# Optimization experiments

Hardware: AMD Instinct MI355X
Metric: run time of the kernel (lower is better)

Reference implementation:

```python
import jax, jax.numpy as jnp
import numpy as np

D_MODEL = 2048
N_HEADS = 16
HEAD_DIM = D_MODEL // N_HEADS
ROPE_BASE = 10000.0
B, T = 2, 2048


def setup_inputs() -> dict:
    key = jax.random.key(0)
    k1, k2, k3 = jax.random.split(key, 3)
    s_in = 1.0 / np.sqrt(D_MODEL)
    x = jax.random.normal(k1, (B, T, D_MODEL), dtype=jnp.float32)
    Wqkv = jax.random.normal(k2, (3 * D_MODEL, D_MODEL), dtype=jnp.float32) * s_in
    bqkv = jnp.zeros((3 * D_MODEL,), dtype=jnp.float32)
    Wo = jax.random.normal(k3, (D_MODEL, D_MODEL), dtype=jnp.float32) * s_in
    bo = jnp.zeros((D_MODEL,), dtype=jnp.float32)
    return {"x": x, "Wqkv": Wqkv, "bqkv": bqkv, "Wo": Wo, "bo": bo}


def _rotate_half(x):
    # [x1,x2,x3,x4] -> [-x2,x1,-x4,x3] (interleaved pairs)
    x_even = x[..., 0::2]
    x_odd = x[..., 1::2]
    return jnp.stack((-x_odd, x_even), axis=-1).reshape(x.shape)


def _rope_cos_sin(seq_len, dtype):
    half = HEAD_DIM // 2
    inv_freq = 1.0 / (ROPE_BASE ** (jnp.arange(half, dtype=jnp.float32) / half))
    freqs = jnp.arange(seq_len, dtype=jnp.float32)[:, None] * inv_freq[None, :]  # (T, half)
    emb = jnp.repeat(freqs, 2, axis=-1)  # (T, D) interleaved
    cos = jnp.cos(emb).astype(dtype)[None, None]  # (1,1,T,D)
    sin = jnp.sin(emb).astype(dtype)[None, None]
    return cos, sin


def reference(x, Wqkv, bqkv, Wo, bo):
    b, t, c = x.shape
    qkv = jnp.einsum('btc,fc->btf', x, Wqkv) + bqkv  # (B,T,3C)
    q, k, v = jnp.split(qkv, 3, axis=-1)
    def to_heads(z):
        return z.reshape(b, t, N_HEADS, HEAD_DIM).transpose(0, 2, 1, 3)  # (B,H,T,D)
    q, k, v = to_heads(q), to_heads(k), to_heads(v)
    cos, sin = _rope_cos_sin(t, x.dtype)
    q = q * cos + _rotate_half(q) * sin
    k = k * cos + _rotate_half(k) * sin
    scale = 1.0 / jnp.sqrt(jnp.asarray(HEAD_DIM, dtype=x.dtype))
    scores = jnp.einsum('bhqd,bhkd->bhqk', q, k) * scale  # (B,H,T,T)
    causal = jnp.tril(jnp.ones((t, t), dtype=bool))
    scores = jnp.where(causal, scores, jnp.finfo(scores.dtype).min)
    attn = jax.nn.softmax(scores, axis=-1)
    out = jnp.einsum('bhqk,bhkd->bhqd', attn, v)  # (B,H,T,D)
    out = out.transpose(0, 2, 1, 3).reshape(b, t, c)
    return jnp.einsum('btc,oc->bto', out, Wo) + bo
```

## Files before the change

### kernel.cpp

```cpp
#include <hip/hip_runtime.h>

using f16 = _Float16;
typedef _Float16 h8 __attribute__((ext_vector_type(8)));
typedef _Float16 h4 __attribute__((ext_vector_type(4)));
typedef float f4 __attribute__((ext_vector_type(4)));
typedef unsigned int u32;
typedef unsigned long long u64;

#define DEVI static __device__ __forceinline__

DEVI f4 mfma16(h8 a, h8 b, f4 c) {
  return __builtin_amdgcn_mfma_f32_16x16x32_f16(a, b, c, 0, 0, 0);
}

DEVI void gl_lds16(const f16* g, f16* l) {
  __builtin_amdgcn_global_load_lds(
      (const __attribute__((address_space(1))) u32*)g,
      (__attribute__((address_space(3))) u32*)l, 16, 0, 0);
}

DEVI u32 pkh2(float a, float b) {
  union { f16 h[2]; u32 u; } x;
  x.h[0] = (f16)a; x.h[1] = (f16)b;
  return x.u;
}

typedef float fv4 __attribute__((ext_vector_type(4)));

__global__ __launch_bounds__(256) void k_cvt(const float* __restrict__ in,
                                             f16* __restrict__ out, int n4) {
  int i = blockIdx.x * 256 + threadIdx.x;
  if (i >= n4) return;
  fv4 v = ((const fv4*)in)[i];
  h4 o;
  o[0] = (f16)v[0]; o[1] = (f16)v[1]; o[2] = (f16)v[2]; o[3] = (f16)v[3];
  ((h4*)out)[i] = o;
}

__global__ __launch_bounds__(256) void k_rope_tbl(float* __restrict__ tbl) {
  int i = blockIdx.x * 256 + threadIdx.x;
  int t = i >> 6, d = i & 63;
  float invf = exp2f(-(float)d * (13.287712379549449f / 64.f));
  float a = (float)t * invf;
  tbl[2 * i]     = cosf(a);
  tbl[2 * i + 1] = sinf(a);
}

template <int F32OUT>
__global__ __launch_bounds__(512, 2) void k_gemm256(const f16* __restrict__ A,
                                                    const f16* __restrict__ Bt,
                                                    const float* __restrict__ bias,
                                                    void* __restrict__ Cp,
                                                    int M, int N, int K, int gy) {
  __shared__ f16 lds[2][32768];
  const int tid = threadIdx.x;
  const int w = tid >> 6, lane = tid & 63;
  const int g = lane >> 4, colq = lane & 15;
  const int wr = w >> 2, wc = w & 3;
  const int sw = (colq >> 1) & 3;
  const int rdc = (g ^ sw) << 3;

  const int nwg = gridDim.x;
  const int q8 = nwg >> 3;
  const int swz = (blockIdx.x & 7) * q8 + (blockIdx.x >> 3);
  const int bm = swz % gy, bn = swz / gy;

  const f16* Ab = A + (size_t)bm * 256 * K;
  const f16* Bb = Bt + (size_t)bn * 256 * K;
  const int nt = K >> 6;

  const int srow = lane >> 2;
  const int schunk = (lane & 3) ^ ((lane >> 3) & 3);

  auto STAGE_A = [&](int kt, int h, f16* buf) {
    const int k0 = (kt << 6) + (h << 5);
#pragma unroll
    for (int j = 0; j < 2; ++j) {
      const int r = (w * 2 + j) * 16;
      gl_lds16(Ab + (size_t)(r + srow) * K + k0 + schunk * 8, buf + h * 8192 + r * 32);
    }
  };
  auto STAGE_B = [&](int kt, int h, f16* buf) {
    const int k0 = (kt << 6) + (h << 5);
#pragma unroll
    for (int j = 0; j < 2; ++j) {
      const int r = (w * 2 + j) * 16;
      gl_lds16(Bb + (size_t)(r + srow) * K + k0 + schunk * 8, buf + 16384 + h * 8192 + r * 32);
    }
  };

  f4 acc[8][4] = {};

  auto LDA = [&](h8* dst, int mh, int h, const f16* cur) {
#pragma unroll
    for (int m = 0; m < 4; ++m) {
      const int row = wr * 128 + (mh * 4 + m) * 16 + colq;
      dst[m] = *(const h8*)(cur + h * 8192 + row * 32 + rdc);
    }
  };
  auto LDB = [&](h8* dst, int h, const f16* cur) {
#pragma unroll
    for (int n = 0; n < 4; ++n) {
      const int row = wc * 64 + n * 16 + colq;
      dst[n] = *(const h8*)(cur + 16384 + h * 8192 + row * 32 + rdc);
    }
  };
  auto MM = [&](h8* af, h8* bf, int mh) {
#pragma unroll
    for (int m = 0; m < 4; ++m)
#pragma unroll
      for (int n = 0; n < 4; ++n)
        acc[mh * 4 + m][n] = mfma16(af[m], bf[n], acc[mh * 4 + m][n]);
  };

  STAGE_A(0, 0, lds[0]); STAGE_B(0, 0, lds[0]);
  STAGE_A(0, 1, lds[0]); STAGE_B(0, 1, lds[0]);
  STAGE_A(1, 0, lds[1]); STAGE_B(1, 0, lds[1]);
  asm volatile("s_waitcnt vmcnt(4)" ::: "memory");
  __builtin_amdgcn_s_barrier();

  for (int t = 0; t < nt; ++t) {
    f16* cur = lds[t & 1];
    f16* nxt = lds[(t & 1) ^ 1];
    const bool m1 = (t + 1 < nt), m2 = (t + 2 < nt);
    h8 af[4], bf[4];
    LDA(af, 0, 0, cur);
    LDB(bf, 0, cur);
    if (m1) STAGE_A(t + 1, 1, nxt);
    __builtin_amdgcn_s_barrier();
    asm volatile("s_waitcnt lgkmcnt(0)" ::: "memory");
    __builtin_amdgcn_sched_barrier(0);
    __builtin_amdgcn_s_setprio(1);
    MM(af, bf, 0);
    __builtin_amdgcn_s_setprio(0);
    __builtin_amdgcn_s_barrier();
    LDA(af, 1, 0, cur);
    if (m1) STAGE_B(t + 1, 1, nxt);
    __builtin_amdgcn_s_barrier();
    asm volatile("s_waitcnt lgkmcnt(0)" ::: "memory");
    __builtin_amdgcn_sched_barrier(0);
    __builtin_amdgcn_s_setprio(1);
    MM(af, bf, 1);
    __builtin_amdgcn_s_setprio(0);
    __builtin_amdgcn_s_barrier();
    LDA(af, 0, 1, cur);
    LDB(bf, 1, cur);
    if (m2) STAGE_A(t + 2, 0, cur);
    __builtin_amdgcn_s_barrier();
    asm volatile("s_waitcnt lgkmcnt(0)" ::: "memory");
    __builtin_amdgcn_sched_barrier(0);
    __builtin_amdgcn_s_setprio(1);
    MM(af, bf, 0);
    __builtin_amdgcn_s_setprio(0);
    __builtin_amdgcn_s_barrier();
    LDA(af, 1, 1, cur);
    if (m2) STAGE_B(t + 2, 0, cur);
    __builtin_amdgcn_s_barrier();
    asm volatile("s_waitcnt lgkmcnt(0)" ::: "memory");
    __builtin_amdgcn_sched_barrier(0);
    __builtin_amdgcn_s_setprio(1);
    MM(af, bf, 1);
    __builtin_amdgcn_s_setprio(0);
    if (m2) {
      asm volatile("s_waitcnt vmcnt(4)" ::: "memory");
    } else {
      asm volatile("s_waitcnt vmcnt(0)" ::: "memory");
    }
    __builtin_amdgcn_s_barrier();
  }

#pragma unroll
  for (int n = 0; n < 4; ++n) {
    const int col = bn * 256 + wc * 64 + n * 16 + colq;
    const float bv = bias[col];
#pragma unroll
    for (int m = 0; m < 8; ++m) {
      const int row0 = bm * 256 + wr * 128 + m * 16 + 4 * g;
#pragma unroll
      for (int r = 0; r < 4; ++r) {
        float v = acc[m][n][r] + bv;
        if constexpr (F32OUT) {
          ((float*)Cp)[(size_t)(row0 + r) * N + col] = v;
        } else {
          ((f16*)Cp)[(size_t)(row0 + r) * N + col] = (f16)v;
        }
      }
    }
  }
}

__global__ __launch_bounds__(256) void k_rope(const f16* __restrict__ qkv,
                                              const float* __restrict__ tbl,
                                              f16* __restrict__ Q, f16* __restrict__ K) {
  int i = blockIdx.x * 256 + threadIdx.x;
  int d = i & 63;
  int h = (i >> 6) & 15;
  int bt = i >> 10;
  int t = bt & 2047;
  int bh = ((bt >> 11) << 4) | h;
  union { u32 u; f16 h2[2]; } qa, ka, qo, ko;
  qa.u = *(const u32*)(qkv + (size_t)bt * 6144 + h * 128 + 2 * d);
  ka.u = *(const u32*)(qkv + (size_t)bt * 6144 + 2048 + h * 128 + 2 * d);
  float c = tbl[2 * (t * 64 + d)];
  float s = tbl[2 * (t * 64 + d) + 1];
  float q0f = (float)qa.h2[0], q1f = (float)qa.h2[1];
  float k0f = (float)ka.h2[0], k1f = (float)ka.h2[1];
  const float SQ = 0.088388347648318447f * 1.4426950408889634f;
  qo.h2[0] = (f16)((q0f * c - q1f * s) * SQ);
  qo.h2[1] = (f16)((q1f * c + q0f * s) * SQ);
  ko.h2[0] = (f16)(k0f * c - k1f * s);
  ko.h2[1] = (f16)(k1f * c + k0f * s);
  *(u32*)(Q + ((size_t)bh * 2048 + t) * 128 + 2 * d) = qo.u;
  *(u32*)(K + ((size_t)bh * 2048 + t) * 128 + 2 * d) = ko.u;
}

__global__ __launch_bounds__(256) void k_vtrans(const f16* __restrict__ qkv,
                                                f16* __restrict__ Vt) {
  __shared__ f16 ldsT[128 * 40];
  const int bh = blockIdx.y, t0 = blockIdx.x * 32;
  const int b = bh >> 4, h = bh & 15;
  const int tid = threadIdx.x;
#pragma unroll
  for (int cc = 0; cc < 2; ++cc) {
    int task = tid + cc * 256;
    int row = task >> 4;
    int ch = task & 15;
    h8 v = *(const h8*)(qkv + (size_t)(b * 2048 + t0 + row) * 6144 + 4096 + h * 128 + ch * 8);
#pragma unroll
    for (int j = 0; j < 8; ++j) ldsT[(ch * 8 + j) * 40 + row] = v[j];
  }
  __syncthreads();
  int d = tid >> 1, seg = tid & 1;
  h8 v0 = *(const h8*)(ldsT + d * 40 + seg * 16);
  h8 v1 = *(const h8*)(ldsT + d * 40 + seg * 16 + 8);
  f16* dst = Vt + ((size_t)bh * 128 + d) * 2048 + t0 + seg * 16;
  *(h8*)dst = v0;
  *(h8*)(dst + 8) = v1;
}

DEVI void stage_tiles(const f16* __restrict__ Kg, const f16* __restrict__ Vtg,
                      f16* bufK, f16* bufV, int kv, int w, int lane) {
#pragma unroll
  for (int jj = 0; jj < 4; ++jj) {
    const int j = w * 4 + jj;
    const int rK = j * 4 + (lane >> 4);
    const int cK = (lane & 15) ^ ((rK & 7) << 1);
    gl_lds16(Kg + (size_t)(kv + rK) * 128 + cK * 8, bufK + j * 512);
    const int rV = j * 8 + (lane >> 3);
    const int cV = (lane & 7) ^ (rV & 7);
    gl_lds16(Vtg + (size_t)rV * 2048 + kv + cV * 8, bufV + j * 512);
  }
}

__global__ __launch_bounds__(256, 1) void k_attn(const f16* __restrict__ Q,
                                                 const f16* __restrict__ K,
                                                 const f16* __restrict__ Vt,
                                                 f16* __restrict__ O) {
  __shared__ f16 lds[2][16384];
  const int tid = threadIdx.x;
  const int w = tid >> 6, lane = tid & 63;
  const int g = lane >> 4, q = lane & 15;
  const int bid = blockIdx.x;
  const int bh = bid & 31;
  const int b = bid >> 5;

  const f16* Kg = K + (size_t)bh * 2048 * 128;
  const f16* Vtg = Vt + (size_t)bh * 128 * 2048;
  const int qx2 = (q & 7) << 1;
  const int qx = q & 7;

  for (int ph = 0; ph < 2; ++ph) {
    const int p = ph ? (15 - b) : b;
    const int q0w = p * 128 + w * 32;
    const int nit = 2 * (p + 1);

    h8 qf[2][4];
#pragma unroll
    for (int set = 0; set < 2; ++set)
#pragma unroll
      for (int d4 = 0; d4 < 4; ++d4)
        qf[set][d4] = *(const h8*)(Q + ((size_t)bh * 2048 + q0w + 16 * set + q) * 128 + d4 * 32 + g * 8);

    stage_tiles(Kg, Vtg, lds[0], lds[0] + 8192, 0, w, lane);
    asm volatile("s_waitcnt vmcnt(0)" ::: "memory");
    __builtin_amdgcn_s_barrier();

    f4 ot[2][8] = {};
    float mrun[2] = {-3.0e38f, -3.0e38f};
    float lrun[2] = {0.f, 0.f};

    for (int it = 0; it < nit; ++it) {
      const int kv0 = it * 64;
      f16* bufK = lds[it & 1];
      f16* bufV = bufK + 8192;
      if (it + 1 < nit) {
        f16* nb = lds[(it + 1) & 1];
        stage_tiles(Kg, Vtg, nb, nb + 8192, kv0 + 64, w, lane);
      }
      if (kv0 < q0w + 32) {
        f4 st[2][4] = {{{0.f,0.f,0.f,0.f},{0.f,0.f,0.f,0.f},{0.f,0.f,0.f,0.f},{0.f,0.f,0.f,0.f}},
                       {{0.f,0.f,0.f,0.f},{0.f,0.f,0.f,0.f},{0.f,0.f,0.f,0.f},{0.f,0.f,0.f,0.f}}};
#pragma unroll
        for (int d4 = 0; d4 < 4; ++d4) {
          h8 kf[4];
#pragma unroll
          for (int s = 0; s < 4; ++s)
            kf[s] = *(const h8*)(bufK + ((16 * s + q) * 16 + ((4 * d4 + g) ^ qx2)) * 8);
#pragma unroll
          for (int set = 0; set < 2; ++set)
#pragma unroll
            for (int s = 0; s < 4; ++s)
              st[set][s] = mfma16(kf[s], qf[set][d4], st[set][s]);
        }
        if (kv0 + 63 > q0w) {
#pragma unroll
          for (int set = 0; set < 2; ++set) {
            const int qcol = q0w + 16 * set + q;
#pragma unroll
            for (int s = 0; s < 4; ++s)
#pragma unroll
              for (int r = 0; r < 4; ++r)
                if (kv0 + s * 16 + 4 * g + r > qcol) st[set][s][r] = -3.0e38f;
          }
        }
        float pm[2];
#pragma unroll
        for (int set = 0; set < 2; ++set) {
          float m0 = st[set][0][0];
#pragma unroll
          for (int s = 0; s < 4; ++s)
#pragma unroll
            for (int r = 0; r < 4; ++r) m0 = fmaxf(m0, st[set][s][r]);
          m0 = fmaxf(m0, __shfl_xor(m0, 16));
          m0 = fmaxf(m0, __shfl_xor(m0, 32));
          pm[set] = m0;
        }
        const bool ok = (pm[0] <= mrun[0] + 8.0f) && (pm[1] <= mrun[1] + 8.0f);
        if (!__all(ok)) {
#pragma unroll
          for (int set = 0; set < 2; ++set) {
            float mnew = fmaxf(mrun[set], pm[set]);
            float corr = exp2f(mrun[set] - mnew);
            lrun[set] *= corr;
#pragma unroll
            for (int dt = 0; dt < 8; ++dt) ot[set][dt] *= corr;
            mrun[set] = mnew;
          }
        }
#pragma unroll
        for (int set = 0; set < 2; ++set) {
          float ps = 0.f;
#pragma unroll
          for (int s = 0; s < 4; ++s)
#pragma unroll
            for (int r = 0; r < 4; ++r) {
              st[set][s][r] = exp2f(st[set][s][r] - mrun[set]);
              ps += st[set][s][r];
            }
          ps += __shfl_xor(ps, 16);
          ps += __shfl_xor(ps, 32);
          lrun[set] += ps;
        }
        union { u32 u[4]; h8 h; } pb[2][2];
        const int s0l = ((g & 1) << 5) | q;
        const bool hi = g >= 2;
#pragma unroll
        for (int set = 0; set < 2; ++set)
#pragma unroll
          for (int hh = 0; hh < 2; ++hh) {
            u32 wA0 = pkh2(st[set][2 * hh][0], st[set][2 * hh][1]);
            u32 wB0 = pkh2(st[set][2 * hh][2], st[set][2 * hh][3]);
            u32 wA1 = pkh2(st[set][2 * hh + 1][0], st[set][2 * hh + 1][1]);
            u32 wB1 = pkh2(st[set][2 * hh + 1][2], st[set][2 * hh + 1][3]);
            u32 a0 = (u32)__shfl((int)wA0, s0l),      a1 = (u32)__shfl((int)wA1, s0l);
            u32 b0 = (u32)__shfl((int)wB0, s0l),      b1 = (u32)__shfl((int)wB1, s0l);
            u32 c0 = (u32)__shfl((int)wA0, s0l + 16), c1 = (u32)__shfl((int)wA1, s0l + 16);
            u32 d0 = (u32)__shfl((int)wB0, s0l + 16), d1 = (u32)__shfl((int)wB1, s0l + 16);
            pb[set][hh].u[0] = hi ? a1 : a0;
            pb[set][hh].u[1] = hi ? b1 : b0;
            pb[set][hh].u[2] = hi ? c1 : c0;
            pb[set][hh].u[3] = hi ? d1 : d0;
          }
#pragma unroll
        for (int hh = 0; hh < 2; ++hh)
#pragma unroll
          for (int dt = 0; dt < 8; ++dt) {
            h8 vf = *(const h8*)(bufV + ((dt * 16 + q) * 8 + ((4 * hh + g) ^ qx)) * 8);
#pragma unroll
            for (int set = 0; set < 2; ++set)
              ot[set][dt] = mfma16(vf, pb[set][hh].h, ot[set][dt]);
          }
      }
      asm volatile("s_waitcnt vmcnt(0)" ::: "memory");
      __builtin_amdgcn_s_barrier();
    }

#pragma unroll
    for (int set = 0; set < 2; ++set) {
      float linv = 1.0f / lrun[set];
      f16* Ob = O + ((size_t)(bh >> 4) * 2048 + q0w + 16 * set + q) * 2048 + (bh & 15) * 128 + 4 * g;
#pragma unroll
      for (int dt = 0; dt < 8; ++dt) {
        union { f16 hh4[4]; u64 u; } o;
#pragma unroll
        for (int r = 0; r < 4; ++r) o.hh4[r] = (f16)(ot[set][dt][r] * linv);
        *(u64*)(Ob + dt * 16) = o.u;
      }
    }
  }
}

extern "C" void kernel_launch(void* const* d_in, const int* in_sizes, int n_in,
                              void* d_out, int out_size, void* d_ws, size_t ws_size,
                              hipStream_t stream) {
  (void)in_sizes; (void)n_in; (void)out_size; (void)ws_size;
  const float* x    = (const float*)d_in[0];
  const float* Wqkv = (const float*)d_in[1];
  const float* bqkv = (const float*)d_in[2];
  const float* Wo   = (const float*)d_in[3];
  const float* bo   = (const float*)d_in[4];

  char* ws = (char*)d_ws;
  f16* xb    = (f16*)ws; ws += (size_t)4096 * 2048 * 2;
  f16* wqkvb = (f16*)ws; ws += (size_t)6144 * 2048 * 2;
  f16* wob   = (f16*)ws; ws += (size_t)2048 * 2048 * 2;
  f16* qkvb  = (f16*)ws; ws += (size_t)4096 * 6144 * 2;
  f16* Qb    = (f16*)ws; ws += (size_t)32 * 2048 * 128 * 2;
  f16* Kb    = (f16*)ws; ws += (size_t)32 * 2048 * 128 * 2;
  f16* Vtb   = (f16*)ws; ws += (size_t)32 * 128 * 2048 * 2;
  f16* attb  = (f16*)ws; ws += (size_t)4096 * 2048 * 2;
  float* tbl = (float*)ws; ws += (size_t)2048 * 64 * 2 * 4;

  k_cvt<<<8192, 256, 0, stream>>>(x, xb, 2097152);
  k_cvt<<<12288, 256, 0, stream>>>(Wqkv, wqkvb, 3145728);
  k_cvt<<<4096, 256, 0, stream>>>(Wo, wob, 1048576);
  k_rope_tbl<<<512, 256, 0, stream>>>(tbl);

  k_gemm256<0><<<384, 512, 0, stream>>>(xb, wqkvb, bqkv, qkvb, 4096, 6144, 2048, 16);

  k_rope<<<16384, 256, 0, stream>>>(qkvb, tbl, Qb, Kb);
  k_vtrans<<<dim3(64, 32), 256, 0, stream>>>(qkvb, Vtb);

  k_attn<<<256, 256, 0, stream>>>(Qb, Kb, Vtb, attb);

  k_gemm256<1><<<128, 512, 0, stream>>>(attb, wob, bo, d_out, 4096, 2048, 2048, 16);
}
```

Measured before the change: 340.6 us.

## Add 128x256-tile GEMM for output projection and relax LDS waits in QKV GEMM

Adds a new k_gemm128 kernel with 128x256 tiles, a simpler double-buffered global-to-LDS pipeline and an XOR-swizzled LDS layout. It is used for the output projection so the launch grows from 128 to 256 workgroups, which should fill more compute units. Separately, the explicit lgkmcnt(0) waits and sched_barriers before each MFMA phase in k_gemm256 are removed, leaving the compiler free to interleave LDS reads with MFMAs. This relies on compiler-inserted waits for correctness and may change the schedule in unpredictable ways.

After: 326.2 us. -4.2%, faster.

```diff
diff --git a/kernel.cpp b/kernel.cpp
--- a/kernel.cpp
+++ b/kernel.cpp
@@ -128,8 +128,6 @@
     LDB(bf, 0, cur);
     if (m1) STAGE_A(t + 1, 1, nxt);
     __builtin_amdgcn_s_barrier();
-    asm volatile("s_waitcnt lgkmcnt(0)" ::: "memory");
-    __builtin_amdgcn_sched_barrier(0);
     __builtin_amdgcn_s_setprio(1);
     MM(af, bf, 0);
     __builtin_amdgcn_s_setprio(0);
@@ -137,8 +135,6 @@
     LDA(af, 1, 0, cur);
     if (m1) STAGE_B(t + 1, 1, nxt);
     __builtin_amdgcn_s_barrier();
-    asm volatile("s_waitcnt lgkmcnt(0)" ::: "memory");
-    __builtin_amdgcn_sched_barrier(0);
     __builtin_amdgcn_s_setprio(1);
     MM(af, bf, 1);
     __builtin_amdgcn_s_setprio(0);
@@ -147,8 +143,6 @@
     LDB(bf, 1, cur);
     if (m2) STAGE_A(t + 2, 0, cur);
     __builtin_amdgcn_s_barrier();
-    asm volatile("s_waitcnt lgkmcnt(0)" ::: "memory");
-    __builtin_amdgcn_sched_barrier(0);
     __builtin_amdgcn_s_setprio(1);
     MM(af, bf, 0);
     __builtin_amdgcn_s_setprio(0);
@@ -156,8 +150,6 @@
     LDA(af, 1, 1, cur);
     if (m2) STAGE_B(t + 2, 0, cur);
     __builtin_amdgcn_s_barrier();
-    asm volatile("s_waitcnt lgkmcnt(0)" ::: "memory");
-    __builtin_amdgcn_sched_barrier(0);
     __builtin_amdgcn_s_setprio(1);
     MM(af, bf, 1);
     __builtin_amdgcn_s_setprio(0);
@@ -176,6 +168,109 @@
 #pragma unroll
     for (int m = 0; m < 8; ++m) {
       const int row0 = bm * 256 + wr * 128 + m * 16 + 4 * g;
+#pragma unroll
+      for (int r = 0; r < 4; ++r) {
+        float v = acc[m][n][r] + bv;
+        if constexpr (F32OUT) {
+          ((float*)Cp)[(size_t)(row0 + r) * N + col] = v;
+        } else {
+          ((f16*)Cp)[(size_t)(row0 + r) * N + col] = (f16)v;
+        }
+      }
+    }
+  }
+}
+
+template <int F32OUT>
+__global__ __launch_bounds__(512, 2) void k_gemm128(const f16* __restrict__ A,
+                                                    const f16* __restrict__ Bt,
+                                                    const float* __restrict__ bias,
+                                                    void* __restrict__ Cp,
+                                                    int M, int N, int K, int gy) {
+  __shared__ f16 lds[2][24576];
+  const int tid = threadIdx.x;
+  const int w = tid >> 6, lane = tid & 63;
+  const int g = lane >> 4, colq = lane & 15;
+  const int wr = w >> 2, wc = w & 3;
+
+  const int nwg = gridDim.x;
+  const int q8 = nwg >> 3;
+  const int swz = (blockIdx.x & 7) * q8 + (blockIdx.x >> 3);
+  const int bm = swz % gy, bn = swz / gy;
+
+  const f16* Ab = A + (size_t)bm * 128 * K;
+  const f16* Bb = Bt + (size_t)bn * 256 * K;
+
+  const int srow = lane >> 3;
+  const int schunk = (lane & 7) ^ srow;
+  const int nt = K >> 6;
+
+  auto STAGE = [&](int kt, f16* buf) {
+    const int k0 = kt << 6;
+    f16* bA = buf;
+    f16* bB = buf + 128 * 64;
+#pragma unroll
+    for (int j = 0; j < 2; ++j) {
+      const int r = w * 16 + j * 8;
+      gl_lds16(Ab + (size_t)(r + srow) * K + k0 + schunk * 8, bA + r * 64);
+    }
+#pragma unroll
+    for (int j = 0; j < 4; ++j) {
+      const int r = w * 32 + j * 8;
+      gl_lds16(Bb + (size_t)(r + srow) * K + k0 + schunk * 8, bB + r * 64);
+    }
+  };
+
+  STAGE(0, lds[0]);
+  STAGE(1, lds[1]);
+  asm volatile("s_waitcnt vmcnt(6)" ::: "memory");
+  __builtin_amdgcn_s_barrier();
+
+  f4 acc[4][4] = {};
+  const int rowA0 = wr * 64 + colq;
+  const int rowB0 = wc * 64 + colq;
+  const int cq7 = colq & 7;
+
+  for (int t = 0; t < nt; ++t) {
+    f16* cur = lds[t & 1];
+    h8 af[2][4], bf[2][4];
+#pragma unroll
+    for (int kki = 0; kki < 2; ++kki) {
+#pragma unroll
+      for (int m = 0; m < 4; ++m)
+        af[kki][m] = *(const h8*)(cur + (rowA0 + m * 16) * 64 + (((kki * 4 + g) ^ cq7) * 8));
+#pragma unroll
+      for (int n = 0; n < 4; ++n)
+        bf[kki][n] = *(const h8*)(cur + 8192 + (rowB0 + n * 16) * 64 + (((kki * 4 + g) ^ cq7) * 8));
+    }
+    asm volatile("s_waitcnt lgkmcnt(0)" ::: "memory");
+    __builtin_amdgcn_s_barrier();
+    const bool more = (t + 2 < nt);
+    if (more) STAGE(t + 2, cur);
+    __builtin_amdgcn_s_setprio(1);
+#pragma unroll
+    for (int m = 0; m < 4; ++m)
+#pragma unroll
+      for (int n = 0; n < 4; ++n)
+#pragma unroll
+        for (int kki = 0; kki < 2; ++kki)
+          acc[m][n] = mfma16(af[kki][m], bf[kki][n], acc[m][n]);
+    __builtin_amdgcn_s_setprio(0);
+    if (more) {
+      asm volatile("s_waitcnt vmcnt(6)" ::: "memory");
+    } else {
+      asm volatile("s_waitcnt vmcnt(0)" ::: "memory");
+    }
+    __builtin_amdgcn_s_barrier();
+  }
+
+#pragma unroll
+  for (int n = 0; n < 4; ++n) {
+    const int col = bn * 256 + wc * 64 + n * 16 + colq;
+    const float bv = bias[col];
+#pragma unroll
+    for (int m = 0; m < 4; ++m) {
+      const int row0 = bm * 128 + wr * 64 + m * 16 + 4 * g;
 #pragma unroll
       for (int r = 0; r < 4; ++r) {
         float v = acc[m][n][r] + bv;
@@ -443,5 +538,5 @@
 
   k_attn<<<256, 256, 0, stream>>>(Qb, Kb, Vtb, attb);
 
-  k_gemm256<1><<<128, 512, 0, stream>>>(attb, wob, bo, d_out, 4096, 2048, 2048, 16);
-}
+  k_gemm128<1><<<256, 512, 0, stream>>>(attb, wob, bo, d_out, 4096, 2048, 2048, 32);
+}
```
